# Kernel optimization log

Hardware: AMD Instinct MI355X
Metric: run time of the kernel (lower is better)

The kernel has to match this reference:

```python
import jax, jax.numpy as jnp
import numpy as np

N_NODES = 50000
N_EDGES = 1000000
D_FEAT = 512
F_ATTN = 64
SLOPE = 0.2


def setup_inputs() -> dict:
    key = jax.random.key(0)
    ks = jax.random.split(key, 8)
    d_sim = jax.random.normal(ks[0], (N_NODES, D_FEAT), dtype=jnp.float32)
    m_sim = jax.random.normal(ks[1], (N_NODES, D_FEAT), dtype=jnp.float32)
    Wd = jax.random.normal(ks[2], (F_ATTN, D_FEAT), dtype=jnp.float32) * (1.0 / np.sqrt(D_FEAT))
    Wm = jax.random.normal(ks[3], (F_ATTN, D_FEAT), dtype=jnp.float32) * (1.0 / np.sqrt(D_FEAT))
    Wa = jax.random.normal(ks[4], (2 * F_ATTN,), dtype=jnp.float32) * (1.0 / np.sqrt(2 * F_ATTN))
    node_type = jax.random.randint(ks[5], (N_NODES,), 0, 2, dtype=jnp.int32)
    edge_src = jax.random.randint(ks[6], (N_EDGES,), 0, N_NODES, dtype=jnp.int32)
    edge_dst = jax.random.randint(ks[7], (N_EDGES,), 0, N_NODES, dtype=jnp.int32)
    return {"d_sim": d_sim, "m_sim": m_sim, "Wd": Wd, "Wm": Wm, "Wa": Wa,
            "node_type": node_type, "edge_src": edge_src, "edge_dst": edge_dst}


def reference(d_sim, m_sim, Wd, Wm, Wa, node_type, edge_src, edge_dst):
    # Per-node projection, type-dependent (type==1 -> disease fc, type==0 -> miRNA fc).
    # Dropout is 0.0 (identity).
    z_d = d_sim @ Wd.T                      # [N, F]
    z_m = m_sim @ Wm.T                      # [N, F]
    z = jnp.where(node_type[:, None] == 1, z_d, z_m)  # [N, F]

    # Edge attention: a = attn_fc(concat(z_src, z_dst)); split Wa to avoid materializing concat.
    zs = z[edge_src]                        # [E, F]
    e = zs @ Wa[:F_ATTN] + z[edge_dst] @ Wa[F_ATTN:]  # [E]
    e = jax.nn.leaky_relu(e, negative_slope=SLOPE)

    # Segment softmax over incoming edges of each dst node (DGL mailbox softmax).
    emax = jax.ops.segment_max(e, edge_dst, num_segments=N_NODES)  # [N]
    ex = jnp.exp(e - emax[edge_dst])                                # [E]
    denom = jax.ops.segment_sum(ex, edge_dst, num_segments=N_NODES)  # [N]
    alpha = ex / denom[edge_dst]                                    # [E]

    # Weighted neighbor aggregation + elu.
    h = jax.ops.segment_sum(alpha[:, None] * zs, edge_dst, num_segments=N_NODES)  # [N, F]
    return jax.nn.elu(h)
```

## Files before the change

### kernel.cpp

```cpp
#include <hip/hip_runtime.h>
#include <hip/hip_bf16.h>

#define N_NODES 50000
#define N_EDGES 1000000
#define D_FEAT 512
#define F_ATTN 64
#define SLOPE 0.2f
#define CAP 64

typedef __attribute__((ext_vector_type(8))) short short8;
typedef __attribute__((ext_vector_type(4))) float floatx4;

static __device__ __forceinline__ short f2bf(float x) {
    unsigned u = __float_as_uint(x);
    unsigned r = (u + 0x7FFFu + ((u >> 16) & 1u)) >> 16;
    return (short)r;
}

static __device__ __forceinline__ short8 cvt2(float4 x, float4 y) {
    short8 r;
    r[0] = f2bf(x.x); r[1] = f2bf(x.y); r[2] = f2bf(x.z); r[3] = f2bf(x.w);
    r[4] = f2bf(y.x); r[5] = f2bf(y.y); r[6] = f2bf(y.z); r[7] = f2bf(y.w);
    return r;
}

static __device__ __forceinline__ float bfu2f(unsigned short v) {
    return __uint_as_float((unsigned)v << 16);
}

static __device__ __forceinline__ void g2lds16(const void* g, void* l) {
    __builtin_amdgcn_global_load_lds(
        (const __attribute__((address_space(1))) void*)g,
        (__attribute__((address_space(3))) void*)l, 16, 0, 0);
}

__global__ __launch_bounds__(256) void wcvt_kernel(
    const float* __restrict__ Wd, const float* __restrict__ Wm,
    short* __restrict__ Wb)
{
    int i = blockIdx.x * 256 + threadIdx.x;
    int half = F_ATTN * D_FEAT;
    float v = (i < half) ? Wd[i] : Wm[i - half];
    Wb[i] = f2bf(v);
}

__global__ __launch_bounds__(256) void proj_kernel(
    const float* __restrict__ d_sim,
    const float* __restrict__ m_sim,
    const short* __restrict__ Wb,
    const float* __restrict__ Wa,
    const int* __restrict__ node_type,
    __hip_bfloat16* __restrict__ z,
    float* __restrict__ s1, float* __restrict__ s2)
{
    __shared__ char smem[65536];

    const int w      = threadIdx.x >> 6;
    const int lane   = threadIdx.x & 63;
    const int laneLo = lane & 15;
    const int quad   = lane >> 4;
    const int nodeBase = blockIdx.x * 64;

    const float* aP[4];
    #pragma unroll
    for (int i = 0; i < 4; i++) {
        int r = w * 16 + i * 4 + (lane >> 4);
        int arow = nodeBase + r; if (arow >= N_NODES) arow = N_NODES - 1;
        int lc = (lane & 15) ^ (r & 7);
        const float* src = (node_type[arow] == 1) ? d_sim : m_sim;
        aP[i] = src + (size_t)arow * D_FEAT + (lc << 2);
    }
    const short* bP[4];
    #pragma unroll
    for (int i = 0; i < 4; i++) {
        int r = (w * 4 + i) * 8 + (lane >> 3);
        int lc = (lane & 7) ^ (r & 7);
        bP[i] = Wb + (size_t)r * D_FEAT + (lc << 3);
    }

    floatx4 accD[4], accM[4];
    #pragma unroll
    for (int nt = 0; nt < 4; nt++) {
        accD[nt] = (floatx4){0.f, 0.f, 0.f, 0.f};
        accM[nt] = (floatx4){0.f, 0.f, 0.f, 0.f};
    }

    {
        char* b0 = smem;
        #pragma unroll
        for (int i = 0; i < 4; i++)
            g2lds16(aP[i], b0 + (w * 16 + i * 4) * 256);
        #pragma unroll
        for (int i = 0; i < 4; i++)
            g2lds16(bP[i], b0 + 16384 + (w * 4 + i) * 1024);
    }
    __syncthreads();

    const int rA  = w * 16 + laneLo;
    const int rx  = laneLo & 7;

    for (int t = 0; t < 8; t++) {
        if (t < 7) {
            char* nb = smem + ((t + 1) & 1) * 32768;
            int k0 = (t + 1) * 64;
            #pragma unroll
            for (int i = 0; i < 4; i++)
                g2lds16(aP[i] + k0, nb + (w * 16 + i * 4) * 256);
            #pragma unroll
            for (int i = 0; i < 4; i++)
                g2lds16(bP[i] + k0, nb + 16384 + (w * 4 + i) * 1024);
        }
        const char* cb = smem + (t & 1) * 32768;
        #pragma unroll
        for (int ks = 0; ks < 2; ks++) {
            int c0 = ks * 8 + quad * 2;
            float4 a0 = *(const float4*)(cb + rA * 256 + ((c0 ^ rx) << 4));
            float4 a1 = *(const float4*)(cb + rA * 256 + (((c0 + 1) ^ rx) << 4));
            short8 a = cvt2(a0, a1);
            int ch = ks * 4 + quad;
            int sl = (ch ^ rx) << 4;
            #pragma unroll
            for (int nt = 0; nt < 4; nt++) {
                const char* rowD = cb + 16384 + (nt * 16 + laneLo) * 128;
                short8 bD = *(const short8*)(rowD + sl);
                short8 bM = *(const short8*)(rowD + 64 * 128 + sl);
                accD[nt] = __builtin_amdgcn_mfma_f32_16x16x32_bf16(a, bD, accD[nt], 0, 0, 0);
                accM[nt] = __builtin_amdgcn_mfma_f32_16x16x32_bf16(a, bM, accM[nt], 0, 0, 0);
            }
        }
        __syncthreads();
    }

    float wa1[4], wa2[4];
    #pragma unroll
    for (int nt = 0; nt < 4; nt++) {
        wa1[nt] = Wa[nt * 16 + laneLo];
        wa2[nt] = Wa[F_ATTN + nt * 16 + laneLo];
    }

    #pragma unroll
    for (int reg = 0; reg < 4; reg++) {
        int node = nodeBase + w * 16 + quad * 4 + reg;
        bool ok = node < N_NODES;
        int isD = ok ? (node_type[node] == 1) : 0;
        float p1 = 0.f, p2 = 0.f;
        #pragma unroll
        for (int nt = 0; nt < 4; nt++) {
            float v = isD ? accD[nt][reg] : accM[nt][reg];
            if (ok) z[(size_t)node * F_ATTN + nt * 16 + laneLo] = __float2bfloat16(v);
            p1 += v * wa1[nt];
            p2 += v * wa2[nt];
        }
        #pragma unroll
        for (int off = 8; off; off >>= 1) {
            p1 += __shfl_xor(p1, off);
            p2 += __shfl_xor(p2, off);
        }
        if (ok && laneLo == 0) { s1[node] = p1; s2[node] = p2; }
    }
}

__global__ __launch_bounds__(256) void build_kernel(
    const int* __restrict__ edge_src, const int* __restrict__ edge_dst,
    const float* __restrict__ s1, const float* __restrict__ s2,
    int* __restrict__ counts, int2* __restrict__ csr_we)
{
    int e = blockIdx.x * 256 + threadIdx.x;
    if (e < N_EDGES) {
        int d = edge_dst[e];
        int s = edge_src[e];
        int r = atomicAdd(&counts[d], 1);
        float t = s1[s] + s2[d];
        float ev = (t > 0.f) ? t : SLOPE * t;
        if (r < CAP) {
            int2 we; we.x = s; we.y = __float_as_int(__expf(ev));
            csr_we[(d << 6) + r] = we;
        }
    }
}

__global__ __launch_bounds__(256) void agg_kernel(
    const int* __restrict__ counts, const int2* __restrict__ csr_we,
    const __hip_bfloat16* __restrict__ z, float* __restrict__ out)
{
    __shared__ float sW[256];
    __shared__ int   sS[256];
    int wv   = threadIdx.x >> 6;
    int lane = threadIdx.x & 63;
    int node = blockIdx.x * 4 + wv;
    int cnt  = counts[node];
    if (cnt > CAP) cnt = CAP;
    int wbase = wv * 64;
    int fgrp  = (lane & 15) * 4;
    int ep    = lane >> 4;

    int2 we = {0, 0};
    if (lane < cnt) we = csr_we[(node << 6) + lane];
    float wgt = __int_as_float(we.y);
    float l = wgt;
    sW[wbase + lane] = wgt;
    sS[wbase + lane] = we.x;

    float4 h = {0.f, 0.f, 0.f, 0.f};
    for (int j = 0; j < cnt; j += 16) {
        #pragma unroll
        for (int u = 0; u < 16; u += 4) {
            int slot = wbase + j + u + ep;
            float wj = sW[slot];
            int   sj = sS[slot];
            ushort4 zz = *(const ushort4*)((const unsigned short*)z +
                                           (size_t)sj * F_ATTN + fgrp);
            h.x += wj * bfu2f(zz.x);
            h.y += wj * bfu2f(zz.y);
            h.z += wj * bfu2f(zz.z);
            h.w += wj * bfu2f(zz.w);
        }
    }
    #pragma unroll
    for (int off = 16; off <= 32; off <<= 1) {
        h.x += __shfl_xor(h.x, off);
        h.y += __shfl_xor(h.y, off);
        h.z += __shfl_xor(h.z, off);
        h.w += __shfl_xor(h.w, off);
    }
    #pragma unroll
    for (int off = 32; off; off >>= 1) l += __shfl_xor(l, off);

    if (ep == 0) {
        float inv = (cnt > 0) ? 1.f / l : 0.f;
        float4 o;
        float v;
        v = h.x * inv; o.x = (v > 0.f) ? v : (__expf(v) - 1.f);
        v = h.y * inv; o.y = (v > 0.f) ? v : (__expf(v) - 1.f);
        v = h.z * inv; o.z = (v > 0.f) ? v : (__expf(v) - 1.f);
        v = h.w * inv; o.w = (v > 0.f) ? v : (__expf(v) - 1.f);
        *(float4*)(out + (size_t)node * F_ATTN + fgrp) = o;
    }
}

extern "C" void kernel_launch(void* const* d_in, const int* in_sizes, int n_in,
                              void* d_out, int out_size, void* d_ws, size_t ws_size,
                              hipStream_t stream) {
    const float* d_sim = (const float*)d_in[0];
    const float* m_sim = (const float*)d_in[1];
    const float* Wd    = (const float*)d_in[2];
    const float* Wm    = (const float*)d_in[3];
    const float* Wa    = (const float*)d_in[4];
    const int* node_type = (const int*)d_in[5];
    const int* edge_src  = (const int*)d_in[6];
    const int* edge_dst  = (const int*)d_in[7];
    float* out = (float*)d_out;

    char* ws = (char*)d_ws;
    __hip_bfloat16* z  = (__hip_bfloat16*)(ws + 0);
    float* s1          = (float*)(ws + 6400000);
    float* s2          = (float*)(ws + 6600000);
    int*   counts      = (int*)  (ws + 6800000);
    short* Wb          = (short*)(ws + 7000000);
    int2*  csr_we      = (int2*) (ws + 8388608);

    hipMemsetAsync(counts, 0, N_NODES * sizeof(int), stream);

    wcvt_kernel<<<(2 * F_ATTN * D_FEAT) / 256, 256, 0, stream>>>(Wd, Wm, Wb);
    proj_kernel<<<(N_NODES + 63) / 64, 256, 0, stream>>>(
        d_sim, m_sim, Wb, Wa, node_type, z, s1, s2);
    build_kernel<<<(N_EDGES + 255) / 256, 256, 0, stream>>>(
        edge_src, edge_dst, s1, s2, counts, csr_we);
    agg_kernel<<<N_NODES / 4, 256, 0, stream>>>(counts, csr_we, z, out);
}
```

Before: 304.4 us.

## Fuse projection and edge bucketing into one interleaved kernel, defer edge weights

The projection blocks and the CSR-bucketing blocks now run in a single launch, with one projection block interleaved every six blocks so the memory-bound GEMM and the atomic-heavy bucketing overlap. The bucket stores only the source index. The attention weight (leaky-relu and exp of s1[src]+s2[dst]) is computed in the aggregation kernel, which removes the dependency of bucketing on the projection outputs. The counts memset is folded into the weight-conversion kernel, saving one launch. The bucketing blocks still hold 64KB of static LDS each, which may limit occupancy for that part of the grid.

```diff
diff --git a/kernel.cpp b/kernel.cpp
--- a/kernel.cpp
+++ b/kernel.cpp
@@ -7,6 +7,9 @@
 #define F_ATTN 64
 #define SLOPE 0.2f
 #define CAP 64
+#define NPROJ 782
+#define NBUILD 3907
+#define NB_TOT (NPROJ + NBUILD)
 
 typedef __attribute__((ext_vector_type(8))) short short8;
 typedef __attribute__((ext_vector_type(4))) float floatx4;
@@ -36,30 +39,50 @@
 
 __global__ __launch_bounds__(256) void wcvt_kernel(
     const float* __restrict__ Wd, const float* __restrict__ Wm,
-    short* __restrict__ Wb)
+    short* __restrict__ Wb, int* __restrict__ counts)
 {
     int i = blockIdx.x * 256 + threadIdx.x;
     int half = F_ATTN * D_FEAT;
     float v = (i < half) ? Wd[i] : Wm[i - half];
     Wb[i] = f2bf(v);
-}
-
-__global__ __launch_bounds__(256) void proj_kernel(
+    if (i < N_NODES) counts[i] = 0;
+}
+
+__global__ __launch_bounds__(256) void mega_kernel(
     const float* __restrict__ d_sim,
     const float* __restrict__ m_sim,
     const short* __restrict__ Wb,
     const float* __restrict__ Wa,
     const int* __restrict__ node_type,
+    const int* __restrict__ edge_src,
+    const int* __restrict__ edge_dst,
     __hip_bfloat16* __restrict__ z,
-    float* __restrict__ s1, float* __restrict__ s2)
+    float* __restrict__ s1, float* __restrict__ s2,
+    int* __restrict__ counts, int* __restrict__ csr_s)
 {
     __shared__ char smem[65536];
+
+    const int bid = blockIdx.x;
+    const int q6  = bid / 6;
+    const bool isProj = ((bid % 6) == 0) && (q6 < NPROJ);
+
+    if (!isProj) {
+        int npb = (bid + 5) / 6; if (npb > NPROJ) npb = NPROJ;
+        int e = (bid - npb) * 256 + threadIdx.x;
+        if (e < N_EDGES) {
+            int d = edge_dst[e];
+            int s = edge_src[e];
+            int r = atomicAdd(&counts[d], 1);
+            if (r < CAP) csr_s[(d << 6) + r] = s;
+        }
+        return;
+    }
 
     const int w      = threadIdx.x >> 6;
     const int lane   = threadIdx.x & 63;
     const int laneLo = lane & 15;
     const int quad   = lane >> 4;
-    const int nodeBase = blockIdx.x * 64;
+    const int nodeBase = q6 * 64;
 
     const float* aP[4];
     #pragma unroll
@@ -160,27 +183,9 @@
     }
 }
 
-__global__ __launch_bounds__(256) void build_kernel(
-    const int* __restrict__ edge_src, const int* __restrict__ edge_dst,
+__global__ __launch_bounds__(256) void agg_kernel(
+    const int* __restrict__ counts, const int* __restrict__ csr_s,
     const float* __restrict__ s1, const float* __restrict__ s2,
-    int* __restrict__ counts, int2* __restrict__ csr_we)
-{
-    int e = blockIdx.x * 256 + threadIdx.x;
-    if (e < N_EDGES) {
-        int d = edge_dst[e];
-        int s = edge_src[e];
-        int r = atomicAdd(&counts[d], 1);
-        float t = s1[s] + s2[d];
-        float ev = (t > 0.f) ? t : SLOPE * t;
-        if (r < CAP) {
-            int2 we; we.x = s; we.y = __float_as_int(__expf(ev));
-            csr_we[(d << 6) + r] = we;
-        }
-    }
-}
-
-__global__ __launch_bounds__(256) void agg_kernel(
-    const int* __restrict__ counts, const int2* __restrict__ csr_we,
     const __hip_bfloat16* __restrict__ z, float* __restrict__ out)
 {
     __shared__ float sW[256];
@@ -194,12 +199,17 @@
     int fgrp  = (lane & 15) * 4;
     int ep    = lane >> 4;
 
-    int2 we = {0, 0};
-    if (lane < cnt) we = csr_we[(node << 6) + lane];
-    float wgt = __int_as_float(we.y);
+    int   src = 0;
+    float wgt = 0.f;
+    if (lane < cnt) {
+        src = csr_s[(node << 6) + lane];
+        float t = s1[src] + s2[node];
+        float ev = (t > 0.f) ? t : SLOPE * t;
+        wgt = __expf(ev);
+    }
     float l = wgt;
     sW[wbase + lane] = wgt;
-    sS[wbase + lane] = we.x;
+    sS[wbase + lane] = src;
 
     float4 h = {0.f, 0.f, 0.f, 0.f};
     for (int j = 0; j < cnt; j += 16) {
@@ -257,14 +267,11 @@
     float* s2          = (float*)(ws + 6600000);
     int*   counts      = (int*)  (ws + 6800000);
     short* Wb          = (short*)(ws + 7000000);
-    int2*  csr_we      = (int2*) (ws + 8388608);
-
-    hipMemsetAsync(counts, 0, N_NODES * sizeof(int), stream);
-
-    wcvt_kernel<<<(2 * F_ATTN * D_FEAT) / 256, 256, 0, stream>>>(Wd, Wm, Wb);
-    proj_kernel<<<(N_NODES + 63) / 64, 256, 0, stream>>>(
-        d_sim, m_sim, Wb, Wa, node_type, z, s1, s2);
-    build_kernel<<<(N_EDGES + 255) / 256, 256, 0, stream>>>(
-        edge_src, edge_dst, s1, s2, counts, csr_we);
-    agg_kernel<<<N_NODES / 4, 256, 0, stream>>>(counts, csr_we, z, out);
-}
+    int*   csr_s       = (int*)  (ws + 8388608);
+
+    wcvt_kernel<<<(2 * F_ATTN * D_FEAT) / 256, 256, 0, stream>>>(Wd, Wm, Wb, counts);
+    mega_kernel<<<NB_TOT, 256, 0, stream>>>(
+        d_sim, m_sim, Wb, Wa, node_type, edge_src, edge_dst,
+        z, s1, s2, counts, csr_s);
+    agg_kernel<<<N_NODES / 4, 256, 0, stream>>>(counts, csr_s, s1, s2, z, out);
+}
```

Result: no change. 308.6 us (+1.4%).
